# Kernel optimization log

Hardware: AMD Instinct MI355X
Metric: run time of the kernel (lower is better)

The kernel has to match this reference:

```python
import jax, jax.numpy as jnp
import numpy as np

B, L, E, D = 4, 1024, 128, 256
NPOI, EPOI, NH, FF = 10000, 128, 8, 256
HD = D // NH


def layer_norm(x, g, b, eps=1e-5):
    m = x.mean(-1, keepdims=True)
    v = ((x - m) ** 2).mean(-1, keepdims=True)
    return (x - m) / jnp.sqrt(v + eps) * g + b


def leaky_relu(x):
    return jnp.where(x >= 0, x, 0.01 * x)


def tokenize_timestamp(t):
    # t: (..., 2) = [timestamp_sec, delta_sec] -> (..., 4) = [week, hour, minute, d_minute]
    week = t[..., 0] % 604800.0 / 86400.0
    hour = t[..., 0] % 86400.0 / 3600.0
    minute = t[..., 0] % 3600.0 / 60.0
    return jnp.stack([week, hour, minute, t[..., 1] / 60.0], -1)


def pos_encode(pos, d):
    # standard sinusoidal PE evaluated at integer positions `pos`
    freq = jnp.exp(-jnp.log(10000.0) * (2.0 * jnp.arange(d // 2, dtype=jnp.float32)) / d)
    ang = pos[..., None].astype(jnp.float32) * freq  # (..., d/2)
    pe = jnp.zeros(pos.shape + (d,), jnp.float32)
    return pe.at[..., 0::2].set(jnp.sin(ang)).at[..., 1::2].set(jnp.cos(ang))


def setup_inputs():
    ks = iter(jax.random.split(jax.random.key(0), 48))

    def nrm(shape, s=0.02):
        return jax.random.normal(next(ks), shape, jnp.float32) * s

    spatial = jax.random.normal(next(ks), (B, L, 2), jnp.float32) * 10.0
    ts = jax.random.uniform(next(ks), (B, L), jnp.float32, 0.0, 1e6)
    dt = jax.random.uniform(next(ks), (B, L), jnp.float32, 0.0, 3600.0)
    token = jax.random.randint(next(ks), (B, L, 2), 0, 2).astype(jnp.float32)
    iq = jnp.zeros((B, L, 4, 2), jnp.float32)
    iq = iq.at[..., 0, 0].set(spatial[..., 0]).at[..., 1, 0].set(spatial[..., 1])
    iq = iq.at[..., 2, 0].set(ts).at[..., 3, 0].set(dt)
    iq = iq.at[..., 0, 1].set(token[..., 0]).at[..., 2, 1].set(token[..., 1])
    positions = jax.random.randint(next(ks), (B, L, 2), 0, L)
    return dict(
        input_seq=iq, positions=positions,
        poi_coors=jax.random.normal(next(ks), (NPOI, 2), jnp.float32) * 10.0,
        poi_embed_mat=nrm((NPOI, EPOI), 1.0),
        sp_w1=nrm((2, E)), sp_b1=jnp.zeros((E,), jnp.float32),
        sp_w2=nrm((E, D)), sp_b2=jnp.zeros((D,), jnp.float32),
        four_w=nrm((4, E), 1.0), four_b=nrm((4, E), 1.0),
        te_w=nrm((4 * E, D)), te_b=jnp.zeros((D,), jnp.float32),
        poi_ln_g=jnp.ones((EPOI,), jnp.float32), poi_ln_b=jnp.zeros((EPOI,), jnp.float32),
        poi_w=nrm((EPOI, D)), poi_b=jnp.zeros((D,), jnp.float32),
        tok_emb=nrm((6, E), 1.0).at[5].set(0.0),
        tok_ln_g=jnp.ones((E,), jnp.float32), tok_ln_b=jnp.zeros((E,), jnp.float32),
        tok_w=nrm((E, D)), tok_b=jnp.zeros((D,), jnp.float32),
        mha_in_w=nrm((D, 3 * D)), mha_in_b=jnp.zeros((3 * D,), jnp.float32),
        mha_out_w=nrm((D, D)), mha_out_b=jnp.zeros((D,), jnp.float32),
        ln1_g=jnp.ones((D,), jnp.float32), ln1_b=jnp.zeros((D,), jnp.float32),
        ff_w1=nrm((D, FF)), ff_b1=jnp.zeros((FF,), jnp.float32),
        ff_w2=nrm((FF, D)), ff_b2=jnp.zeros((D,), jnp.float32),
        ln2_g=jnp.ones((D,), jnp.float32), ln2_b=jnp.zeros((D,), jnp.float32))


def reference(input_seq, positions, poi_coors, poi_embed_mat,
              sp_w1, sp_b1, sp_w2, sp_b2, four_w, four_b, te_w, te_b,
              poi_ln_g, poi_ln_b, poi_w, poi_b,
              tok_emb, tok_ln_g, tok_ln_b, tok_w, tok_b,
              mha_in_w, mha_in_b, mha_out_w, mha_out_b,
              ln1_g, ln1_b, ff_w1, ff_b1, ff_w2, ff_b2, ln2_g, ln2_b):
    token = input_seq[..., jnp.array([0, 2]), 1].astype(jnp.int32)  # (B,L,2)
    spatial = input_seq[:, :, 0:2, 0]                                # (B,L,2)
    tt = tokenize_timestamp(input_seq[:, :, 2:4, 0])                 # (B,L,4)
    # token embedding: Embedding(6) -> LN -> Linear -> (B,L,2,D)
    tok_e = layer_norm(tok_emb[token], tok_ln_g, tok_ln_b) @ tok_w + tok_b
    # spatial embedding (note: original's masked_fill is non-inplace and discarded)
    sp_e = leaky_relu(spatial @ sp_w1 + sp_b1) @ sp_w2 + sp_b2 + tok_e[:, :, 0]
    # brute-force nearest POI: cdist^2 + argmin + gather
    d2 = ((poi_coors[None, None] - spatial[:, :, None]) ** 2).sum(-1)  # (B,L,NPOI)
    poi = jnp.argmin(d2, -1)                                           # (B,L)
    poi_e = layer_norm(poi_embed_mat[poi], poi_ln_g, poi_ln_b) @ poi_w + poi_b + tok_e[:, :, 0]
    # temporal: 4 FourierEncode modules -> concat -> LeakyReLU -> Linear
    t_e = jnp.cos(tt[..., None] * four_w + four_b).reshape(B, L, 4 * E)
    t_e = leaky_relu(t_e) @ te_w + te_b + tok_e[:, :, 1]
    # modal mixer: 1-layer post-norm TransformerEncoder over the 3 modalities
    x = jnp.stack([sp_e, t_e, poi_e], 2).reshape(B * L, 3, D)
    qkv = x @ mha_in_w + mha_in_b
    q, k, v = jnp.split(qkv, 3, -1)
    q = q.reshape(B * L, 3, NH, HD)
    k = k.reshape(B * L, 3, NH, HD)
    v = v.reshape(B * L, 3, NH, HD)
    att = jax.nn.softmax(jnp.einsum('nqhd,nkhd->nhqk', q, k) / jnp.sqrt(jnp.float32(HD)), -1)
    o = jnp.einsum('nhqk,nkhd->nqhd', att, v).reshape(B * L, 3, D) @ mha_out_w + mha_out_b
    x = layer_norm(x + o, ln1_g, ln1_b)
    x = layer_norm(x + (jax.nn.relu(x @ ff_w1 + ff_b1) @ ff_w2 + ff_b2), ln2_g, ln2_b)
    modal_h = x.reshape(B, L, 3, D).mean(2)
    modal_h = modal_h + pos_encode(positions[..., 0], D) + pos_encode(positions[..., 1], D)
    return modal_h  # == mem_seq in the original forward
```

## Files before the change

kernel.cpp:

```cpp
#include <hip/hip_runtime.h>
#include <math.h>

namespace {
constexpr int E = 128, D = 256;
constexpr int NPOI = 10000, NH = 8, FFD = 256;
constexpr int HD = D / NH;
constexpr int NTOK = 4096;
constexpr int TA = 4;
constexpr float LN_EPS = 1e-5f;

constexpr int PK_QKV = 0;
constexpr int PK_OUT = 196608;
constexpr int PK_FF1 = 262144;
constexpr int PK_FF2 = 327680;
constexpr int PK_E0  = 393216;
constexpr int PK_E1  = 458752;
constexpr int PK_E2  = 622592;
constexpr int PK_TOTAL = 688128;
constexpr int NTILES = PK_TOTAL / 512;
}

using frag8 = __attribute__((ext_vector_type(8))) short;
using f32x4 = __attribute__((ext_vector_type(4))) float;

__device__ __forceinline__ float bf2f(short s) {
    union { unsigned u; float f; } x; x.u = ((unsigned)(unsigned short)s) << 16; return x.f;
}
__device__ __forceinline__ unsigned short f2bf(float f) {
    union { float f; unsigned u; } x; x.f = f;
    unsigned r = x.u + 0x7fffu + ((x.u >> 16) & 1u);
    return (unsigned short)(r >> 16);
}

__device__ __forceinline__ float wsum64(float v) {
#pragma unroll
    for (int m = 1; m < 64; m <<= 1) v += __shfl_xor(v, m);
    return v;
}

__device__ __forceinline__ void ln128_bf(const float* __restrict__ src,
                                         const float* __restrict__ g,
                                         const float* __restrict__ b,
                                         short* __restrict__ dst1,
                                         short* __restrict__ dst2, int lane) {
    float v0 = src[lane], v1 = src[64 + lane];
    float mean = wsum64(v0 + v1) * (1.0f / 128.0f);
    float d0 = v0 - mean, d1 = v1 - mean;
    float var = wsum64(d0 * d0 + d1 * d1) * (1.0f / 128.0f);
    float inv = sqrtf(var + LN_EPS);
    float y0 = d0 / inv * g[lane] + b[lane];
    float y1 = d1 / inv * g[64 + lane] + b[64 + lane];
    unsigned short s0 = f2bf(y0), s1 = f2bf(y1);
    dst1[lane] = (short)s0; dst1[64 + lane] = (short)s1;
    if (dst2) { dst2[lane] = (short)s0; dst2[64 + lane] = (short)s1; }
}

__global__ __launch_bounds__(256)
void pack_weights(const float* __restrict__ wqkv, const float* __restrict__ wout,
                  const float* __restrict__ fw1,  const float* __restrict__ fw2,
                  const float* __restrict__ sp_w2, const float* __restrict__ te_w,
                  const float* __restrict__ poi_w, const float* __restrict__ tok_w,
                  unsigned short* __restrict__ pk)
{
    __shared__ float buf[4][32 * 17];
    const int wv = threadIdx.x >> 6, lane = threadIdx.x & 63;
    const int tile = blockIdx.x * 4 + wv;
    if (tile >= NTILES) return;

    int t = tile, sel, base;
    if (t < 384)              { sel = 0; base = PK_QKV; }
    else if ((t -= 384) < 128){ sel = 1; base = PK_OUT; }
    else if ((t -= 128) < 128){ sel = 2; base = PK_FF1; }
    else if ((t -= 128) < 128){ sel = 3; base = PK_FF2; }
    else if ((t -= 128) < 128){ sel = 4; base = PK_E0; }
    else if ((t -= 128) < 320){ sel = 5; base = PK_E1; }
    else                      { t -= 320; sel = 6; base = PK_E2; }
    const int NKT = (sel == 5) ? 20 : 8;
    const int nt = t / NKT, kt = t % NKT;

    const int k = kt * 32 + (lane >> 1);
    const int n0 = nt * 16 + (lane & 1) * 8;
    const float* row;
    switch (sel) {
        case 0:  row = wqkv + (size_t)k * 768; break;
        case 1:  row = wout + (size_t)k * 256; break;
        case 2:  row = fw1  + (size_t)k * 256; break;
        case 3:  row = fw2  + (size_t)k * 256; break;
        case 4:  row = (k < 128) ? sp_w2 + (size_t)k * 256 : tok_w + (size_t)(k - 128) * 256; break;
        case 5:  row = (k < 512) ? te_w  + (size_t)k * 256 : tok_w + (size_t)(k - 512) * 256; break;
        default: row = (k < 128) ? poi_w + (size_t)k * 256 : tok_w + (size_t)(k - 128) * 256; break;
    }
    float4 v0 = *(const float4*)(row + n0);
    float4 v1 = *(const float4*)(row + n0 + 4);
    float* b = buf[wv];
    const int wb = (lane >> 1) * 17 + (lane & 1) * 8;
    b[wb + 0] = v0.x; b[wb + 1] = v0.y; b[wb + 2] = v0.z; b[wb + 3] = v0.w;
    b[wb + 4] = v1.x; b[wb + 5] = v1.y; b[wb + 6] = v1.z; b[wb + 7] = v1.w;
    __syncthreads();

    const int rb = (lane >> 4) * 8, c = lane & 15;
    frag8 fr;
#pragma unroll
    for (int j = 0; j < 8; ++j) fr[j] = (short)f2bf(b[(rb + j) * 17 + c]);
    *(frag8*)(pk + base + ((size_t)t * 64 + lane) * 8) = fr;
}

__global__ __launch_bounds__(256, 4)
void embed_mfma(const float* __restrict__ iq,
                const float* __restrict__ poi_coors,
                const float* __restrict__ poi_embed,
                const float* __restrict__ sp_w1, const float* __restrict__ sp_b1,
                const float* __restrict__ sp_b2,
                const float* __restrict__ four_w, const float* __restrict__ four_b,
                const float* __restrict__ te_b,
                const float* __restrict__ poi_ln_g, const float* __restrict__ poi_ln_b,
                const float* __restrict__ poi_b,
                const float* __restrict__ tok_emb,
                const float* __restrict__ tok_ln_g, const float* __restrict__ tok_ln_b,
                const float* __restrict__ tok_b,
                const unsigned short* __restrict__ pk,
                unsigned short* __restrict__ xout)
{
    constexpr int P0 = 264, P1 = 648, P2 = 264;
    const int tid = threadIdx.x;
    const int w = tid >> 6, lane = tid & 63;
    const int quad = lane >> 4, l16 = lane & 15;
    const int n0 = blockIdx.x * TA;

    __shared__ __align__(16) char  U[25088];
    __shared__ __align__(16) short s_x[TA * 768];
    __shared__ float s_meta[TA][6];
    __shared__ int   s_tok[TA][2];
    __shared__ float s_wd[4][TA];
    __shared__ int   s_wi[4][TA];
    __shared__ int   s_poi[TA];

    short* h0 = (short*)U;
    short* h1 = (short*)U + 1056;
    short* h2 = (short*)U + 3648;

    if (tid < TA) {
        const float* p = iq + (size_t)(n0 + tid) * 8;
        s_meta[tid][0] = p[0];
        s_meta[tid][1] = p[2];
        float ts = p[4];
        float dt = p[6];
        s_tok[tid][0] = (int)p[1];
        s_tok[tid][1] = (int)p[5];
        s_meta[tid][2] = fmodf(ts, 604800.0f) / 86400.0f;
        s_meta[tid][3] = fmodf(ts, 86400.0f) / 3600.0f;
        s_meta[tid][4] = fmodf(ts, 3600.0f) / 60.0f;
        s_meta[tid][5] = dt / 60.0f;
    }
    __syncthreads();

    {
        float sx[TA], sy[TA], bd[TA];
        int bi[TA];
#pragma unroll
        for (int t = 0; t < TA; ++t) {
            sx[t] = s_meta[t][0]; sy[t] = s_meta[t][1];
            bd[t] = INFINITY; bi[t] = NPOI;
        }
        const float2* pc = (const float2*)poi_coors;
        for (int i = tid; i < NPOI; i += 256) {
            float2 p = pc[i];
#pragma unroll
            for (int t = 0; t < TA; ++t) {
                float dx = __fsub_rn(p.x, sx[t]);
                float dy = __fsub_rn(p.y, sy[t]);
                float d  = __fadd_rn(__fmul_rn(dx, dx), __fmul_rn(dy, dy));
                if (d < bd[t]) { bd[t] = d; bi[t] = i; }
            }
        }
#pragma unroll
        for (int m = 1; m < 64; m <<= 1) {
#pragma unroll
            for (int t = 0; t < TA; ++t) {
                float od = __shfl_xor(bd[t], m);
                int   oi = __shfl_xor(bi[t], m);
                if (od < bd[t] || (od == bd[t] && oi < bi[t])) { bd[t] = od; bi[t] = oi; }
            }
        }
        if (lane == 0) {
#pragma unroll
            for (int t = 0; t < TA; ++t) { s_wd[w][t] = bd[t]; s_wi[w][t] = bi[t]; }
        }
        __syncthreads();
        if (tid < TA) {
            float bdd = s_wd[0][tid]; int bii = s_wi[0][tid];
#pragma unroll
            for (int ww = 1; ww < 4; ++ww) {
                float od = s_wd[ww][tid]; int oi = s_wi[ww][tid];
                if (od < bdd || (od == bdd && oi < bii)) { bdd = od; bii = oi; }
            }
            s_poi[tid] = bii;
        }
        __syncthreads();
    }

    {
        const int t = w;
        ln128_bf(tok_emb + (size_t)s_tok[t][0] * E, tok_ln_g, tok_ln_b,
                 h0 + t * P0 + 128, h2 + t * P2 + 128, lane);
        ln128_bf(tok_emb + (size_t)s_tok[t][1] * E, tok_ln_g, tok_ln_b,
                 h1 + t * P1 + 512, nullptr, lane);
        ln128_bf(poi_embed + (size_t)s_poi[t] * E, poi_ln_g, poi_ln_b,
                 h2 + t * P2, nullptr, lane);
    }

    for (int idx = tid; idx < TA * 128; idx += 256) {
        int t = idx >> 7, l = idx & 127;
        float h = s_meta[t][0] * sp_w1[l] + s_meta[t][1] * sp_w1[128 + l] + sp_b1[l];
        h0[t * P0 + l] = (short)f2bf((h >= 0.0f) ? h : 0.01f * h);
    }
    for (int idx = tid; idx < TA * 512; idx += 256) {
        int t = idx >> 9, jj = idx & 511, f = jj >> 7;
        float c = cosf(s_meta[t][2 + f] * four_w[jj] + four_b[jj]);
        h1[t * P1 + jj] = (short)f2bf((c >= 0.0f) ? c : 0.01f * c);
    }
    __syncthreads();

    {
        f32x4 acc[4];
#pragma unroll
        for (int nt = 0; nt < 4; ++nt) {
            int c = w * 64 + nt * 16 + l16;
            float bv = sp_b2[c] + tok_b[c];
            acc[nt][0] = bv; acc[nt][1] = bv; acc[nt][2] = bv; acc[nt][3] = bv;
        }
        for (int kt = 0; kt < 8; ++kt) {
            frag8 a = *(const frag8*)(&h0[l16 * P0 + kt * 32 + quad * 8]);
#pragma unroll
            for (int nt = 0; nt < 4; ++nt) {
                frag8 b = *(const frag8*)(pk + PK_E0 + (((size_t)(w * 4 + nt) * 8 + kt) * 64 + lane) * 8);
                acc[nt] = __builtin_amdgcn_mfma_f32_16x16x32_bf16(a, b, acc[nt], 0, 0, 0);
            }
        }
        if (quad == 0) {
#pragma unroll
            for (int nt = 0; nt < 4; ++nt)
#pragma unroll
                for (int r = 0; r < 4; ++r)
                    s_x[r * 768 + w * 64 + nt * 16 + l16] = (short)f2bf(acc[nt][r]);
        }
    }
    {
        f32x4 acc[4];
#pragma unroll
        for (int nt = 0; nt < 4; ++nt) {
            int c = w * 64 + nt * 16 + l16;
            float bv = te_b[c] + tok_b[c];
            acc[nt][0] = bv; acc[nt][1] = bv; acc[nt][2] = bv; acc[nt][3] = bv;
        }
        for (int kt = 0; kt < 20; ++kt) {
            frag8 a = *(const frag8*)(&h1[l16 * P1 + kt * 32 + quad * 8]);
#pragma unroll
            for (int nt = 0; nt < 4; ++nt) {
                frag8 b = *(const frag8*)(pk + PK_E1 + (((size_t)(w * 4 + nt) * 20 + kt) * 64 + lane) * 8);
                acc[nt] = __builtin_amdgcn_mfma_f32_16x16x32_bf16(a, b, acc[nt], 0, 0, 0);
            }
        }
        if (quad == 0) {
#pragma unroll
            for (int nt = 0; nt < 4; ++nt)
#pragma unroll
                for (int r = 0; r < 4; ++r)
                    s_x[r * 768 + 256 + w * 64 + nt * 16 + l16] = (short)f2bf(acc[nt][r]);
        }
    }
    {
        f32x4 acc[4];
#pragma unroll
        for (int nt = 0; nt < 4; ++nt) {
            int c = w * 64 + nt * 16 + l16;
            float bv = poi_b[c] + tok_b[c];
            acc[nt][0] = bv; acc[nt][1] = bv; acc[nt][2] = bv; acc[nt][3] = bv;
        }
        for (int kt = 0; kt < 8; ++kt) {
            frag8 a = *(const frag8*)(&h2[l16 * P2 + kt * 32 + quad * 8]);
#pragma unroll
            for (int nt = 0; nt < 4; ++nt) {
                frag8 b = *(const frag8*)(pk + PK_E2 + (((size_t)(w * 4 + nt) * 8 + kt) * 64 + lane) * 8);
                acc[nt] = __builtin_amdgcn_mfma_f32_16x16x32_bf16(a, b, acc[nt], 0, 0, 0);
            }
        }
        if (quad == 0) {
#pragma unroll
            for (int nt = 0; nt < 4; ++nt)
#pragma unroll
                for (int r = 0; r < 4; ++r)
                    s_x[r * 768 + 512 + w * 64 + nt * 16 + l16] = (short)f2bf(acc[nt][r]);
        }
    }
    __syncthreads();

    {
        unsigned short* xg = xout + (size_t)n0 * 768;
        for (int c = tid; c < TA * 96; c += 256)
            *(frag8*)(xg + c * 8) = *(const frag8*)(&s_x[c * 8]);
    }
}

__global__ __launch_bounds__(256, 4)
void mha_ff_mfma(const unsigned short* __restrict__ xin,
                 const unsigned short* __restrict__ pk,
                 const float* __restrict__ bqkv, const float* __restrict__ bout,
                 const float* __restrict__ ln1g, const float* __restrict__ ln1b,
                 const float* __restrict__ fb1,  const float* __restrict__ fb2,
                 const float* __restrict__ ln2g, const float* __restrict__ ln2b,
                 const int* __restrict__ positions,
                 float* __restrict__ out)
{
    constexpr int PA = 264;
    constexpr int PQ = 776;
    constexpr int PF = 260;
    const int tid = threadIdx.x;
    const int w = tid >> 6, lane = tid & 63;
    const int quad = lane >> 4, l16 = lane & 15;
    const int n0tok = blockIdx.x * TA;
    const unsigned short* xg = xin + (size_t)n0tok * 3 * D;

    __shared__ __align__(16) short s_a[16 * PA];
    __shared__ __align__(16) char  U[25088];
    __shared__ float s_att[TA * NH * 9];

    short* qkv = (short*)U;
    float* s_f = (float*)U;
    short* s_h = (short*)(U + 16640);

    for (int i = tid; i < 12 * 32; i += 256) {
        int row = i >> 5, col = (i & 31) * 8;
        *(frag8*)(&s_a[row * PA + col]) = *(const frag8*)(xg + row * 256 + col);
    }
    __syncthreads();

    float xres[16];

    {
        f32x4 acc[12];
#pragma unroll
        for (int nt = 0; nt < 12; ++nt) {
            float bv = bqkv[w * 192 + nt * 16 + l16];
            acc[nt][0] = bv; acc[nt][1] = bv; acc[nt][2] = bv; acc[nt][3] = bv;
        }
        for (int kt = 0; kt < 8; ++kt) {
            frag8 a = *(const frag8*)(&s_a[l16 * PA + kt * 32 + quad * 8]);
#pragma unroll
            for (int nt = 0; nt < 12; ++nt) {
                frag8 b = *(const frag8*)(pk + PK_QKV + (((size_t)(w * 12 + nt) * 8 + kt) * 64 + lane) * 8);
                acc[nt] = __builtin_amdgcn_mfma_f32_16x16x32_bf16(a, b, acc[nt], 0, 0, 0);
            }
        }
#pragma unroll
        for (int nt = 0; nt < 4; ++nt)
#pragma unroll
            for (int r = 0; r < 4; ++r)
                xres[nt * 4 + r] = bf2f(s_a[(quad * 4 + r) * PA + w * 64 + nt * 16 + l16]);
#pragma unroll
        for (int nt = 0; nt < 12; ++nt)
#pragma unroll
            for (int r = 0; r < 4; ++r) {
                int row = quad * 4 + r, col = w * 192 + nt * 16 + l16;
                qkv[row * PQ + col] = (short)f2bf(acc[nt][r]);
            }
    }
    __syncthreads();

    for (int idx3 = tid; idx3 < TA * NH * 3; idx3 += 256) {
        int tok = idx3 / 24, rem = idx3 % 24;
        int h = rem / 3, qr = rem % 3;
        const short* qp = qkv + (tok * 3 + qr) * PQ + h * HD;
        const short* k0 = qkv + (tok * 3 + 0) * PQ + D + h * HD;
        const short* k1 = qkv + (tok * 3 + 1) * PQ + D + h * HD;
        const short* k2 = qkv + (tok * 3 + 2) * PQ + D + h * HD;
        float s0 = 0.0f, s1 = 0.0f, s2 = 0.0f;
#pragma unroll
        for (int u = 0; u < HD; ++u) {
            float q = bf2f(qp[u]);
            s0 += q * bf2f(k0[u]);
            s1 += q * bf2f(k1[u]);
            s2 += q * bf2f(k2[u]);
        }
        const float sc = 1.0f / sqrtf((float)HD);
        s0 *= sc; s1 *= sc; s2 *= sc;
        float m = fmaxf(s0, fmaxf(s1, s2));
        float e0 = expf(s0 - m), e1 = expf(s1 - m), e2 = expf(s2 - m);
        float inv = 1.0f / (e0 + e1 + e2);
        s_att[idx3 * 3 + 0] = e0 * inv;
        s_att[idx3 * 3 + 1] = e1 * inv;
        s_att[idx3 * 3 + 2] = e2 * inv;
    }
    __syncthreads();

    {
        const int h = tid >> 5;
#pragma unroll
        for (int tok = 0; tok < TA; ++tok) {
            float v0 = bf2f(qkv[(tok * 3 + 0) * PQ + 2 * D + tid]);
            float v1 = bf2f(qkv[(tok * 3 + 1) * PQ + 2 * D + tid]);
            float v2 = bf2f(qkv[(tok * 3 + 2) * PQ + 2 * D + tid]);
#pragma unroll
            for (int qr = 0; qr < 3; ++qr) {
                const float* a = s_att + tok * 72 + h * 9 + qr * 3;
                s_a[(tok * 3 + qr) * PA + tid] = (short)f2bf(a[0] * v0 + a[1] * v1 + a[2] * v2);
            }
        }
    }
    __syncthreads();

    {
        f32x4 acc[4];
#pragma unroll
        for (int nt = 0; nt < 4; ++nt) {
            float bv = bout[w * 64 + nt * 16 + l16];
            acc[nt][0] = bv; acc[nt][1] = bv; acc[nt][2] = bv; acc[nt][3] = bv;
        }
        for (int kt = 0; kt < 8; ++kt) {
            frag8 a = *(const frag8*)(&s_a[l16 * PA + kt * 32 + quad * 8]);
#pragma unroll
            for (int nt = 0; nt < 4; ++nt) {
                frag8 b = *(const frag8*)(pk + PK_OUT + (((size_t)(w * 4 + nt) * 8 + kt) * 64 + lane) * 8);
                acc[nt] = __builtin_amdgcn_mfma_f32_16x16x32_bf16(a, b, acc[nt], 0, 0, 0);
            }
        }
        __syncthreads();
#pragma unroll
        for (int nt = 0; nt < 4; ++nt)
#pragma unroll
            for (int r = 0; r < 4; ++r) {
                int row = quad * 4 + r, col = w * 64 + nt * 16 + l16;
                s_f[row * PF + col] = acc[nt][r] + xres[nt * 4 + r];
            }
    }
    __syncthreads();

#pragma unroll
    for (int rr = 0; rr < 4; ++rr) {
        int row = w + rr * 4, col = lane * 4;
        float4 v = *(const float4*)(&s_f[row * PF + col]);
        float mean = wsum64(v.x + v.y + v.z + v.w) * (1.0f / 256.0f);
        float dx = v.x - mean, dy = v.y - mean, dz = v.z - mean, dw = v.w - mean;
        float var = wsum64(dx * dx + dy * dy + dz * dz + dw * dw) * (1.0f / 256.0f);
        float s = sqrtf(var + LN_EPS);
        float4 g = *(const float4*)(ln1g + col), b = *(const float4*)(ln1b + col);
        float y0 = dx / s * g.x + b.x, y1 = dy / s * g.y + b.y;
        float y2 = dz / s * g.z + b.z, y3 = dw / s * g.w + b.w;
        float4 yv; yv.x = y0; yv.y = y1; yv.z = y2; yv.w = y3;
        *(float4*)(&s_f[row * PF + col]) = yv;
        ushort4 bb; bb.x = f2bf(y0); bb.y = f2bf(y1); bb.z = f2bf(y2); bb.w = f2bf(y3);
        *(ushort4*)(&s_a[row * PA + col]) = bb;
    }
    __syncthreads();

    {
        f32x4 acc[4];
#pragma unroll
        for (int nt = 0; nt < 4; ++nt) {
            float bv = fb1[w * 64 + nt * 16 + l16];
            acc[nt][0] = bv; acc[nt][1] = bv; acc[nt][2] = bv; acc[nt][3] = bv;
        }
        for (int kt = 0; kt < 8; ++kt) {
            frag8 a = *(const frag8*)(&s_a[l16 * PA + kt * 32 + quad * 8]);
#pragma unroll
            for (int nt = 0; nt < 4; ++nt) {
                frag8 b = *(const frag8*)(pk + PK_FF1 + (((size_t)(w * 4 + nt) * 8 + kt) * 64 + lane) * 8);
                acc[nt] = __builtin_amdgcn_mfma_f32_16x16x32_bf16(a, b, acc[nt], 0, 0, 0);
            }
        }
#pragma unroll
        for (int nt = 0; nt < 4; ++nt)
#pragma unroll
            for (int r = 0; r < 4; ++r) {
                int row = quad * 4 + r, col = w * 64 + nt * 16 + l16;
                s_h[row * PA + col] = (short)f2bf(fmaxf(acc[nt][r], 0.0f));
            }
    }
    __syncthreads();

    {
        f32x4 acc[4];
#pragma unroll
        for (int nt = 0; nt < 4; ++nt) {
            float bv = fb2[w * 64 + nt * 16 + l16];
            acc[nt][0] = bv; acc[nt][1] = bv; acc[nt][2] = bv; acc[nt][3] = bv;
        }
        for (int kt = 0; kt < 8; ++kt) {
            frag8 a = *(const frag8*)(&s_h[l16 * PA + kt * 32 + quad * 8]);
#pragma unroll
            for (int nt = 0; nt < 4; ++nt) {
                frag8 b = *(const frag8*)(pk + PK_FF2 + (((size_t)(w * 4 + nt) * 8 + kt) * 64 + lane) * 8);
                acc[nt] = __builtin_amdgcn_mfma_f32_16x16x32_bf16(a, b, acc[nt], 0, 0, 0);
            }
        }
#pragma unroll
        for (int nt = 0; nt < 4; ++nt)
#pragma unroll
            for (int r = 0; r < 4; ++r) {
                int row = quad * 4 + r, col = w * 64 + nt * 16 + l16;
                float y = s_f[row * PF + col];
                s_f[row * PF + col] = acc[nt][r] + y;
            }
    }
    __syncthreads();

#pragma unroll
    for (int rr = 0; rr < 4; ++rr) {
        int row = w + rr * 4, col = lane * 4;
        float4 v = *(const float4*)(&s_f[row * PF + col]);
        float mean = wsum64(v.x + v.y + v.z + v.w) * (1.0f / 256.0f);
        float dx = v.x - mean, dy = v.y - mean, dz = v.z - mean, dw = v.w - mean;
        float var = wsum64(dx * dx + dy * dy + dz * dz + dw * dw) * (1.0f / 256.0f);
        float s = sqrtf(var + LN_EPS);
        float4 g = *(const float4*)(ln2g + col), b = *(const float4*)(ln2b + col);
        float4 zv;
        zv.x = dx / s * g.x + b.x; zv.y = dy / s * g.y + b.y;
        zv.z = dz / s * g.z + b.z; zv.w = dw / s * g.w + b.w;
        *(float4*)(&s_f[row * PF + col]) = zv;
    }
    __syncthreads();

    {
        const int fi = tid >> 1;
        const float freq = expf(-logf(10000.0f) * (2.0f * fi) / (float)D);
#pragma unroll
        for (int t = 0; t < TA; ++t) {
            int n = n0tok + t;
            float m3 = (s_f[(3 * t) * PF + tid] + s_f[(3 * t + 1) * PF + tid] +
                        s_f[(3 * t + 2) * PF + tid]) / 3.0f;
            float p0 = (float)positions[2 * n], p1 = (float)positions[2 * n + 1];
            float a0 = p0 * freq, a1 = p1 * freq;
            float pe = (tid & 1) ? (cosf(a0) + cosf(a1)) : (sinf(a0) + sinf(a1));
            out[(size_t)n * D + tid] = m3 + pe;
        }
    }
}

extern "C" void kernel_launch(void* const* d_in, const int* in_sizes, int n_in,
                              void* d_out, int out_size, void* d_ws, size_t ws_size,
                              hipStream_t stream)
{
    const float* iq        = (const float*)d_in[0];
    const int*   positions = (const int*)d_in[1];
    const float* poi_coors = (const float*)d_in[2];
    const float* poi_embed = (const float*)d_in[3];
    const float* sp_w1     = (const float*)d_in[4];
    const float* sp_b1     = (const float*)d_in[5];
    const float* sp_w2     = (const float*)d_in[6];
    const float* sp_b2     = (const float*)d_in[7];
    const float* four_w    = (const float*)d_in[8];
    const float* four_b    = (const float*)d_in[9];
    const float* te_w      = (const float*)d_in[10];
    const float* te_b      = (const float*)d_in[11];
    const float* poi_ln_g  = (const float*)d_in[12];
    const float* poi_ln_b  = (const float*)d_in[13];
    const float* poi_w     = (const float*)d_in[14];
    const float* poi_b     = (const float*)d_in[15];
    const float* tok_emb   = (const float*)d_in[16];
    const float* tok_ln_g  = (const float*)d_in[17];
    const float* tok_ln_b  = (const float*)d_in[18];
    const float* tok_w     = (const float*)d_in[19];
    const float* tok_b     = (const float*)d_in[20];
    const float* mha_in_w  = (const float*)d_in[21];
    const float* mha_in_b  = (const float*)d_in[22];
    const float* mha_out_w = (const float*)d_in[23];
    const float* mha_out_b = (const float*)d_in[24];
    const float* ln1_g     = (const float*)d_in[25];
    const float* ln1_b     = (const float*)d_in[26];
    const float* ff_w1     = (const float*)d_in[27];
    const float* ff_b1     = (const float*)d_in[28];
    const float* ff_w2     = (const float*)d_in[29];
    const float* ff_b2     = (const float*)d_in[30];
    const float* ln2_g     = (const float*)d_in[31];
    const float* ln2_b     = (const float*)d_in[32];

    unsigned short* pkw = (unsigned short*)d_ws;
    unsigned short* xws = (unsigned short*)((char*)d_ws + PK_TOTAL * 2);

    pack_weights<<<NTILES / 4, 256, 0, stream>>>(
        mha_in_w, mha_out_w, ff_w1, ff_w2, sp_w2, te_w, poi_w, tok_w, pkw);

    embed_mfma<<<NTOK / TA, 256, 0, stream>>>(
        iq, poi_coors, poi_embed, sp_w1, sp_b1, sp_b2, four_w, four_b, te_b,
        poi_ln_g, poi_ln_b, poi_b, tok_emb, tok_ln_g, tok_ln_b, tok_b,
        pkw, xws);

    mha_ff_mfma<<<NTOK / TA, 256, 0, stream>>>(
        xws, pkw, mha_in_b, mha_out_b, ln1_g, ln1_b,
        ff_b1, ff_b2, ln2_g, ln2_b, positions, (float*)d_out);
}
```

Before: 211.7 us.

## Retile embed kernel to 16-token groups split across four column blocks

The embedding kernel now processes 16 tokens per group, so the 16-row MFMA tiles are fully occupied instead of holding only 4 real rows. Each of four blocks in a group computes a 64-column slice and writes bf16 results straight to global memory, dropping the shared staging buffer. The trade-off is that every block repeats the nearest-POI search, the layer norms and the Fourier features for all 16 tokens, which quadruples that per-token work across the grid. Launch bounds on both kernels drop from 4 to 3 blocks per SM to fit the larger shared buffers.

```diff
diff --git a/kernel.cpp b/kernel.cpp
--- a/kernel.cpp
+++ b/kernel.cpp
@@ -6,7 +6,8 @@
 constexpr int NPOI = 10000, NH = 8, FFD = 256;
 constexpr int HD = D / NH;
 constexpr int NTOK = 4096;
-constexpr int TA = 4;
+constexpr int TB = 4;
+constexpr int TG = 16;
 constexpr float LN_EPS = 1e-5f;
 
 constexpr int PK_QKV = 0;
@@ -105,7 +106,7 @@
     *(frag8*)(pk + base + ((size_t)t * 64 + lane) * 8) = fr;
 }
 
-__global__ __launch_bounds__(256, 4)
+__global__ __launch_bounds__(256, 3)
 void embed_mfma(const float* __restrict__ iq,
                 const float* __restrict__ poi_coors,
                 const float* __restrict__ poi_embed,
@@ -125,21 +126,21 @@
     const int tid = threadIdx.x;
     const int w = tid >> 6, lane = tid & 63;
     const int quad = lane >> 4, l16 = lane & 15;
-    const int n0 = blockIdx.x * TA;
-
-    __shared__ __align__(16) char  U[25088];
-    __shared__ __align__(16) short s_x[TA * 768];
-    __shared__ float s_meta[TA][6];
-    __shared__ int   s_tok[TA][2];
-    __shared__ float s_wd[4][TA];
-    __shared__ int   s_wi[4][TA];
-    __shared__ int   s_poi[TA];
-
-    short* h0 = (short*)U;
-    short* h1 = (short*)U + 1056;
-    short* h2 = (short*)U + 3648;
-
-    if (tid < TA) {
+    const int g = blockIdx.x >> 2, ns = blockIdx.x & 3;
+    const int n0 = g * TG;
+    const int ntg = ns * 4 + w;
+    const int c0 = ntg * 16 + l16;
+
+    __shared__ __align__(16) short s_h0[16 * P0];
+    __shared__ __align__(16) short s_h1[16 * P1];
+    __shared__ __align__(16) short s_h2[16 * P2];
+    __shared__ float s_meta[TG][6];
+    __shared__ int   s_tok[TG][2];
+    __shared__ float s_wd[4][4];
+    __shared__ int   s_wi[4][4];
+    __shared__ int   s_poi[TG];
+
+    if (tid < TG) {
         const float* p = iq + (size_t)(n0 + tid) * 8;
         s_meta[tid][0] = p[0];
         s_meta[tid][1] = p[2];
@@ -154,19 +155,19 @@
     }
     __syncthreads();
 
-    {
-        float sx[TA], sy[TA], bd[TA];
-        int bi[TA];
-#pragma unroll
-        for (int t = 0; t < TA; ++t) {
-            sx[t] = s_meta[t][0]; sy[t] = s_meta[t][1];
+    for (int ch = 0; ch < 4; ++ch) {
+        float sx[4], sy[4], bd[4];
+        int bi[4];
+#pragma unroll
+        for (int t = 0; t < 4; ++t) {
+            sx[t] = s_meta[ch * 4 + t][0]; sy[t] = s_meta[ch * 4 + t][1];
             bd[t] = INFINITY; bi[t] = NPOI;
         }
         const float2* pc = (const float2*)poi_coors;
         for (int i = tid; i < NPOI; i += 256) {
             float2 p = pc[i];
 #pragma unroll
-            for (int t = 0; t < TA; ++t) {
+            for (int t = 0; t < 4; ++t) {
                 float dx = __fsub_rn(p.x, sx[t]);
                 float dy = __fsub_rn(p.y, sy[t]);
                 float d  = __fadd_rn(__fmul_rn(dx, dx), __fmul_rn(dy, dy));
@@ -176,7 +177,7 @@
 #pragma unroll
         for (int m = 1; m < 64; m <<= 1) {
 #pragma unroll
-            for (int t = 0; t < TA; ++t) {
+            for (int t = 0; t < 4; ++t) {
                 float od = __shfl_xor(bd[t], m);
                 int   oi = __shfl_xor(bi[t], m);
                 if (od < bd[t] || (od == bd[t] && oi < bi[t])) { bd[t] = od; bi[t] = oi; }
@@ -184,125 +185,83 @@
         }
         if (lane == 0) {
 #pragma unroll
-            for (int t = 0; t < TA; ++t) { s_wd[w][t] = bd[t]; s_wi[w][t] = bi[t]; }
+            for (int t = 0; t < 4; ++t) { s_wd[w][t] = bd[t]; s_wi[w][t] = bi[t]; }
         }
         __syncthreads();
-        if (tid < TA) {
+        if (tid < 4) {
             float bdd = s_wd[0][tid]; int bii = s_wi[0][tid];
 #pragma unroll
             for (int ww = 1; ww < 4; ++ww) {
                 float od = s_wd[ww][tid]; int oi = s_wi[ww][tid];
                 if (od < bdd || (od == bdd && oi < bii)) { bdd = od; bii = oi; }
             }
-            s_poi[tid] = bii;
+            s_poi[ch * 4 + tid] = bii;
         }
         __syncthreads();
     }
 
-    {
-        const int t = w;
+#pragma unroll
+    for (int k4 = 0; k4 < 4; ++k4) {
+        const int t = w + k4 * 4;
         ln128_bf(tok_emb + (size_t)s_tok[t][0] * E, tok_ln_g, tok_ln_b,
-                 h0 + t * P0 + 128, h2 + t * P2 + 128, lane);
+                 s_h0 + t * P0 + 128, s_h2 + t * P2 + 128, lane);
         ln128_bf(tok_emb + (size_t)s_tok[t][1] * E, tok_ln_g, tok_ln_b,
-                 h1 + t * P1 + 512, nullptr, lane);
+                 s_h1 + t * P1 + 512, nullptr, lane);
         ln128_bf(poi_embed + (size_t)s_poi[t] * E, poi_ln_g, poi_ln_b,
-                 h2 + t * P2, nullptr, lane);
-    }
-
-    for (int idx = tid; idx < TA * 128; idx += 256) {
+                 s_h2 + t * P2, nullptr, lane);
+    }
+
+    for (int idx = tid; idx < TG * 128; idx += 256) {
         int t = idx >> 7, l = idx & 127;
         float h = s_meta[t][0] * sp_w1[l] + s_meta[t][1] * sp_w1[128 + l] + sp_b1[l];
-        h0[t * P0 + l] = (short)f2bf((h >= 0.0f) ? h : 0.01f * h);
-    }
-    for (int idx = tid; idx < TA * 512; idx += 256) {
+        s_h0[t * P0 + l] = (short)f2bf((h >= 0.0f) ? h : 0.01f * h);
+    }
+    for (int idx = tid; idx < TG * 512; idx += 256) {
         int t = idx >> 9, jj = idx & 511, f = jj >> 7;
         float c = cosf(s_meta[t][2 + f] * four_w[jj] + four_b[jj]);
-        h1[t * P1 + jj] = (short)f2bf((c >= 0.0f) ? c : 0.01f * c);
-    }
-    __syncthreads();
-
-    {
-        f32x4 acc[4];
-#pragma unroll
-        for (int nt = 0; nt < 4; ++nt) {
-            int c = w * 64 + nt * 16 + l16;
-            float bv = sp_b2[c] + tok_b[c];
-            acc[nt][0] = bv; acc[nt][1] = bv; acc[nt][2] = bv; acc[nt][3] = bv;
-        }
+        s_h1[t * P1 + jj] = (short)f2bf((c >= 0.0f) ? c : 0.01f * c);
+    }
+    __syncthreads();
+
+    {
+        float bv = sp_b2[c0] + tok_b[c0];
+        f32x4 acc; acc[0] = bv; acc[1] = bv; acc[2] = bv; acc[3] = bv;
         for (int kt = 0; kt < 8; ++kt) {
-            frag8 a = *(const frag8*)(&h0[l16 * P0 + kt * 32 + quad * 8]);
-#pragma unroll
-            for (int nt = 0; nt < 4; ++nt) {
-                frag8 b = *(const frag8*)(pk + PK_E0 + (((size_t)(w * 4 + nt) * 8 + kt) * 64 + lane) * 8);
-                acc[nt] = __builtin_amdgcn_mfma_f32_16x16x32_bf16(a, b, acc[nt], 0, 0, 0);
-            }
-        }
-        if (quad == 0) {
-#pragma unroll
-            for (int nt = 0; nt < 4; ++nt)
-#pragma unroll
-                for (int r = 0; r < 4; ++r)
-                    s_x[r * 768 + w * 64 + nt * 16 + l16] = (short)f2bf(acc[nt][r]);
-        }
-    }
-    {
-        f32x4 acc[4];
-#pragma unroll
-        for (int nt = 0; nt < 4; ++nt) {
-            int c = w * 64 + nt * 16 + l16;
-            float bv = te_b[c] + tok_b[c];
-            acc[nt][0] = bv; acc[nt][1] = bv; acc[nt][2] = bv; acc[nt][3] = bv;
-        }
+            frag8 a = *(const frag8*)(&s_h0[l16 * P0 + kt * 32 + quad * 8]);
+            frag8 b = *(const frag8*)(pk + PK_E0 + (((size_t)ntg * 8 + kt) * 64 + lane) * 8);
+            acc = __builtin_amdgcn_mfma_f32_16x16x32_bf16(a, b, acc, 0, 0, 0);
+        }
+#pragma unroll
+        for (int r = 0; r < 4; ++r)
+            xout[(size_t)(n0 + quad * 4 + r) * 768 + c0] = f2bf(acc[r]);
+    }
+    {
+        float bv = te_b[c0] + tok_b[c0];
+        f32x4 acc; acc[0] = bv; acc[1] = bv; acc[2] = bv; acc[3] = bv;
         for (int kt = 0; kt < 20; ++kt) {
-            frag8 a = *(const frag8*)(&h1[l16 * P1 + kt * 32 + quad * 8]);
-#pragma unroll
-            for (int nt = 0; nt < 4; ++nt) {
-                frag8 b = *(const frag8*)(pk + PK_E1 + (((size_t)(w * 4 + nt) * 20 + kt) * 64 + lane) * 8);
-                acc[nt] = __builtin_amdgcn_mfma_f32_16x16x32_bf16(a, b, acc[nt], 0, 0, 0);
-            }
-        }
-        if (quad == 0) {
-#pragma unroll
-            for (int nt = 0; nt < 4; ++nt)
-#pragma unroll
-                for (int r = 0; r < 4; ++r)
-                    s_x[r * 768 + 256 + w * 64 + nt * 16 + l16] = (short)f2bf(acc[nt][r]);
-        }
-    }
-    {
-        f32x4 acc[4];
-#pragma unroll
-        for (int nt = 0; nt < 4; ++nt) {
-            int c = w * 64 + nt * 16 + l16;
-            float bv = poi_b[c] + tok_b[c];
-            acc[nt][0] = bv; acc[nt][1] = bv; acc[nt][2] = bv; acc[nt][3] = bv;
-        }
+            frag8 a = *(const frag8*)(&s_h1[l16 * P1 + kt * 32 + quad * 8]);
+            frag8 b = *(const frag8*)(pk + PK_E1 + (((size_t)ntg * 20 + kt) * 64 + lane) * 8);
+            acc = __builtin_amdgcn_mfma_f32_16x16x32_bf16(a, b, acc, 0, 0, 0);
+        }
+#pragma unroll
+        for (int r = 0; r < 4; ++r)
+            xout[(size_t)(n0 + quad * 4 + r) * 768 + 256 + c0] = f2bf(acc[r]);
+    }
+    {
+        float bv = poi_b[c0] + tok_b[c0];
+        f32x4 acc; acc[0] = bv; acc[1] = bv; acc[2] = bv; acc[3] = bv;
         for (int kt = 0; kt < 8; ++kt) {
-            frag8 a = *(const frag8*)(&h2[l16 * P2 + kt * 32 + quad * 8]);
-#pragma unroll
-            for (int nt = 0; nt < 4; ++nt) {
-                frag8 b = *(const frag8*)(pk + PK_E2 + (((size_t)(w * 4 + nt) * 8 + kt) * 64 + lane) * 8);
-                acc[nt] = __builtin_amdgcn_mfma_f32_16x16x32_bf16(a, b, acc[nt], 0, 0, 0);
-            }
-        }
-        if (quad == 0) {
-#pragma unroll
-            for (int nt = 0; nt < 4; ++nt)
-#pragma unroll
-                for (int r = 0; r < 4; ++r)
-                    s_x[r * 768 + 512 + w * 64 + nt * 16 + l16] = (short)f2bf(acc[nt][r]);
-        }
-    }
-    __syncthreads();
-
-    {
-        unsigned short* xg = xout + (size_t)n0 * 768;
-        for (int c = tid; c < TA * 96; c += 256)
-            *(frag8*)(xg + c * 8) = *(const frag8*)(&s_x[c * 8]);
-    }
-}
-
-__global__ __launch_bounds__(256, 4)
+            frag8 a = *(const frag8*)(&s_h2[l16 * P2 + kt * 32 + quad * 8]);
+            frag8 b = *(const frag8*)(pk + PK_E2 + (((size_t)ntg * 8 + kt) * 64 + lane) * 8);
+            acc = __builtin_amdgcn_mfma_f32_16x16x32_bf16(a, b, acc, 0, 0, 0);
+        }
+#pragma unroll
+        for (int r = 0; r < 4; ++r)
+            xout[(size_t)(n0 + quad * 4 + r) * 768 + 512 + c0] = f2bf(acc[r]);
+    }
+}
+
+__global__ __launch_bounds__(256, 3)
 void mha_ff_mfma(const unsigned short* __restrict__ xin,
                  const unsigned short* __restrict__ pk,
                  const float* __restrict__ bqkv, const float* __restrict__ bout,
@@ -318,12 +277,12 @@
     const int tid = threadIdx.x;
     const int w = tid >> 6, lane = tid & 63;
     const int quad = lane >> 4, l16 = lane & 15;
-    const int n0tok = blockIdx.x * TA;
+    const int n0tok = blockIdx.x * TB;
     const unsigned short* xg = xin + (size_t)n0tok * 3 * D;
 
     __shared__ __align__(16) short s_a[16 * PA];
     __shared__ __align__(16) char  U[25088];
-    __shared__ float s_att[TA * NH * 9];
+    __shared__ float s_att[TB * NH * 9];
 
     short* qkv = (short*)U;
     float* s_f = (float*)U;
@@ -367,7 +326,7 @@
     }
     __syncthreads();
 
-    for (int idx3 = tid; idx3 < TA * NH * 3; idx3 += 256) {
+    for (int idx3 = tid; idx3 < TB * NH * 3; idx3 += 256) {
         int tok = idx3 / 24, rem = idx3 % 24;
         int h = rem / 3, qr = rem % 3;
         const short* qp = qkv + (tok * 3 + qr) * PQ + h * HD;
@@ -396,7 +355,7 @@
     {
         const int h = tid >> 5;
 #pragma unroll
-        for (int tok = 0; tok < TA; ++tok) {
+        for (int tok = 0; tok < TB; ++tok) {
             float v0 = bf2f(qkv[(tok * 3 + 0) * PQ + 2 * D + tid]);
             float v1 = bf2f(qkv[(tok * 3 + 1) * PQ + 2 * D + tid]);
             float v2 = bf2f(qkv[(tok * 3 + 2) * PQ + 2 * D + tid]);
@@ -524,7 +483,7 @@
         const int fi = tid >> 1;
         const float freq = expf(-logf(10000.0f) * (2.0f * fi) / (float)D);
 #pragma unroll
-        for (int t = 0; t < TA; ++t) {
+        for (int t = 0; t < TB; ++t) {
             int n = n0tok + t;
             float m3 = (s_f[(3 * t) * PF + tid] + s_f[(3 * t + 1) * PF + tid] +
                         s_f[(3 * t + 2) * PF + tid]) / 3.0f;
@@ -580,12 +539,12 @@
     pack_weights<<<NTILES / 4, 256, 0, stream>>>(
         mha_in_w, mha_out_w, ff_w1, ff_w2, sp_w2, te_w, poi_w, tok_w, pkw);
 
-    embed_mfma<<<NTOK / TA, 256, 0, stream>>>(
+    embed_mfma<<<(NTOK / TG) * 4, 256, 0, stream>>>(
         iq, poi_coors, poi_embed, sp_w1, sp_b1, sp_b2, four_w, four_b, te_b,
         poi_ln_g, poi_ln_b, poi_b, tok_emb, tok_ln_g, tok_ln_b, tok_b,
         pkw, xws);
 
-    mha_ff_mfma<<<NTOK / TA, 256, 0, stream>>>(
+    mha_ff_mfma<<<NTOK / TB, 256, 0, stream>>>(
         xws, pkw, mha_in_b, mha_out_b, ln1_g, ln1_b,
         ff_b1, ff_b2, ln2_g, ln2_b, positions, (float*)d_out);
 }
```

Measured after the change: 235.0 us. +11.0%, slower.
